# Optimization experiments

Hardware: AMD Instinct MI355X
Metric: run time of the kernel (lower is better)

The kernel has to match this reference:

```python
import jax, jax.numpy as jnp
import numpy as np

B_, L, DM = 4, 1024, 1024
DI, DS, DR, DC = 1024, 16, 64, 4
NH = 4
DK = DM // NH


def setup_inputs() -> dict:
    key = jax.random.key(0)
    ks = jax.random.split(key, 16)
    def w(i, shape, scale=0.02):
        return jax.random.normal(ks[i], shape, dtype=jnp.float32) * scale
    inp = {
        "x": jax.random.normal(ks[0], (B_, L, DM), dtype=jnp.float32),
        "xx": jax.random.normal(ks[1], (B_, L, DI), dtype=jnp.float32),
        "in_proj_w": w(2, (DI, DM)),
        "conv_w": w(3, (DI, 1, DC)),            # depthwise conv, groups=DI
        "conv_b": jnp.zeros((DI,), jnp.float32),
        "x_proj_w": w(4, (DR + 2 * DS, DI)),
        "dt_proj_w": w(5, (DI, DR)),
        "dt_proj_b": jnp.zeros((DI,), jnp.float32),
        "A_log": jnp.log(jnp.tile(jnp.arange(1, DS + 1, dtype=jnp.float32)[None, :], (DI, 1))),
        "D": jnp.ones((DI,), jnp.float32),
        "wq": w(6, (DM, DM)), "bq": jnp.zeros((DM,), jnp.float32),
        "wk": w(7, (DM, DM)), "bk": jnp.zeros((DM,), jnp.float32),
        "wv": w(8, (DM, DM)), "bv": jnp.zeros((DM,), jnp.float32),
        "wo": w(9, (DM, DM)), "bo": jnp.zeros((DM,), jnp.float32),
    }
    return inp


def _stim_forward(x, xx, in_proj_w, conv_w, conv_b, x_proj_w, dt_proj_w, dt_proj_b,
                  A_log, D, wq, bq, wk, bk, wv, bv, wo, bo):
    b, l, _ = xx.shape
    # query branch: in_proj (Linear, no bias)
    q = x @ in_proj_w.T                                    # (b, l, DI)
    # kv branch: causal depthwise conv1d (padding d_conv-1, truncated to l)
    xc = jnp.transpose(xx, (0, 2, 1))                      # (b, DI, l)
    xc = jax.lax.conv_general_dilated(
        xc, conv_w, window_strides=(1,), padding=[(DC - 1, 0)],
        dimension_numbers=("NCH", "OIH", "NCH"), feature_group_count=DI)
    xc = xc + conv_b[None, :, None]
    u = jax.nn.silu(jnp.transpose(xc, (0, 2, 1)))          # (b, l, DI)
    # SSM parameter projections
    A = -jnp.exp(A_log)                                    # (DI, DS)
    x_dbl = u @ x_proj_w.T                                 # (b, l, DR+2*DS)
    delta, Bm, Cm = jnp.split(x_dbl, [DR, DR + DS], axis=-1)
    delta = jax.nn.softplus(delta @ dt_proj_w.T + dt_proj_b)  # (b, l, DI)
    deltaA = jnp.exp(jnp.einsum("bld,dn->bldn", delta, A))    # (b, l, DI, DS)
    deltaBu = jnp.einsum("bld,bln,bld->bldn", delta, Bm, u)   # (b, l, DI, DS)
    # selective scan over time
    def step(h, inp):
        dA_t, dBu_t, C_t = inp
        h = dA_t * h + dBu_t                               # (b, DI, DS)
        y_t = jnp.einsum("bdn,bn->bd", h, C_t)             # (b, DI)
        return h, y_t
    h0 = jnp.zeros((b, DI, DS), dtype=u.dtype)
    _, ys = jax.lax.scan(step, h0, (jnp.moveaxis(deltaA, 1, 0),
                                    jnp.moveaxis(deltaBu, 1, 0),
                                    jnp.moveaxis(Cm, 1, 0)))
    y = jnp.moveaxis(ys, 0, 1) + u * D                     # (b, l, DI)
    # cross attention: query = q, key/value = y
    Q = (q @ wq.T + bq).reshape(b, l, NH, DK).transpose(0, 2, 1, 3)
    K = (y @ wk.T + bk).reshape(b, l, NH, DK).transpose(0, 2, 1, 3)
    V = (y @ wv.T + bv).reshape(b, l, NH, DK).transpose(0, 2, 1, 3)
    scale = 1.0 / np.sqrt(DK).astype(np.float32)
    scores = jnp.einsum("bhqd,bhkd->bhqk", Q, K) * scale
    attn = jax.nn.softmax(scores, axis=-1)
    out = jnp.einsum("bhqk,bhkd->bhqd", attn, V)
    out = out.transpose(0, 2, 1, 3).reshape(b, l, DM)
    return out @ wo.T + bo


def reference(x, xx, in_proj_w, conv_w, conv_b, x_proj_w, dt_proj_w, dt_proj_b,
              A_log, D, wq, bq, wk, bk, wv, bv, wo, bo):
    return _stim_forward(x, xx, in_proj_w, conv_w, conv_b, x_proj_w, dt_proj_w,
                         dt_proj_b, A_log, D, wq, bq, wk, bk, wv, bv, wo, bo)
```

## Files before the change

### kernel.cpp

```cpp
#include <hip/hip_runtime.h>
#include <math.h>

#define B_  4
#define L_  1024
#define DM  1024
#define DI  1024
#define DS  16
#define DR  64
#define DCV 4
#define NH  4
#define DK  256

#define NCH 32
#define CHL (L_ / NCH)

typedef __attribute__((ext_vector_type(8))) short short8;
typedef __attribute__((ext_vector_type(4))) float floatx4;

static __device__ __forceinline__ unsigned short f2bf(float f) {
    unsigned int u = __float_as_uint(f);
    u += 0x7fffu + ((u >> 16) & 1u);
    return (unsigned short)(u >> 16);
}
static __device__ __forceinline__ float bf2f(unsigned short s) {
    return __uint_as_float(((unsigned int)s) << 16);
}

#define GLL(gp, lp) __builtin_amdgcn_global_load_lds( \
        (const __attribute__((address_space(1))) void*)(gp), \
        (__attribute__((address_space(3))) void*)(lp), 16, 0, 0)

struct PrepArgs {
    const float* xx; const float* cw; const float* cb;
    float* u; unsigned short* ub;
    const float* xs; unsigned short* xd;
    const float* s[7]; unsigned short* d[7];
    int n[7];
    int ns[7];
};

__global__ __launch_bounds__(256) void prep(PrepArgs pa)
{
    int bid = blockIdx.x, tid = threadIdx.x;
    if (bid < 16384) {
        int idx = bid * 256 + tid;
        int d = idx & (DI - 1);
        int l = (idx >> 10) & (L_ - 1);
        int b = idx >> 20;
        const float* xb = pa.xx + (size_t)b * L_ * DI + d;
        float z = pa.cb[d];
#pragma unroll
        for (int j = 0; j < DCV; j++) {
            int t = l - (DCV - 1) + j;
            if (t >= 0) z += xb[(size_t)t * DI] * pa.cw[d * DCV + j];
        }
        float v = z / (1.0f + __expf(-z));
        pa.u[idx] = v;
        pa.ub[idx] = f2bf(v);
        return;
    }
    bid -= 16384;
    if (bid < 4096) {
        int i = (bid * 256 + tid) * 4;
        float4 v = *(const float4*)(pa.xs + i);
        ushort4 o;
        o.x = f2bf(v.x); o.y = f2bf(v.y); o.z = f2bf(v.z); o.w = f2bf(v.w);
        *(ushort4*)(pa.xd + i) = o;
        return;
    }
    bid -= 4096;
#pragma unroll
    for (int r = 0; r < 7; r++) {
        int nb = pa.n[r] >> 10;
        if (bid < nb) {
            int i = (bid * 256 + tid) * 4;
            int ns = pa.ns[r];
            const float* s = pa.s[r];
            ushort4 o;
            if (i + 4 <= ns) {
                float4 v = *(const float4*)(s + i);
                o.x = f2bf(v.x); o.y = f2bf(v.y); o.z = f2bf(v.z); o.w = f2bf(v.w);
            } else {
                float v[4];
#pragma unroll
                for (int j = 0; j < 4; j++) v[j] = (i + j < ns) ? s[i + j] : 0.f;
                o.x = f2bf(v[0]); o.y = f2bf(v[1]); o.z = f2bf(v[2]); o.w = f2bf(v[3]);
            }
            *(ushort4*)(pa.d[r] + i) = o;
            return;
        }
        bid -= nb;
    }
}

struct GDesc {
    const unsigned short* A;
    const unsigned short* W;
    const float* bias;
    float* Cf;
    unsigned short* Cb;
    int K, lda, ldw, ldc, ldc2;
    int mode;
    float scale;
    int gx, gy;
};
struct GArgs { GDesc g[3]; };

__global__ __launch_bounds__(256) void gemm_multi(GArgs ga)
{
    GDesc g = ga.g[blockIdx.z];
    if ((int)blockIdx.x >= g.gx || (int)blockIdx.y >= g.gy) return;

    __shared__ __align__(16) unsigned short Asm[2][128 * 32];
    __shared__ __align__(16) unsigned short Bsm[2][128 * 32];

    int tid = threadIdx.x;
    int wid = tid >> 6;
    int lane = tid & 63;
    int wm = wid & 1, wn = wid >> 1;
    int lr = lane & 15, quad = lane >> 4;

    const unsigned short* Ab = g.A + (size_t)blockIdx.y * 128 * g.lda;
    const unsigned short* Wb = g.W + (size_t)blockIdx.x * 128 * g.ldw;

    int srow = tid >> 2;
    int scol = (tid & 3) * 8;
    const unsigned short* Ap = Ab + (size_t)srow * g.lda + scol;
    const unsigned short* Wp = Wb + (size_t)srow * g.ldw + scol;

    int lbase = (wid * 16) * 32;

    floatx4 acc[4][4];
#pragma unroll
    for (int i = 0; i < 4; i++)
#pragma unroll
        for (int j = 0; j < 4; j++) acc[i][j] = (floatx4){0.f, 0.f, 0.f, 0.f};

    GLL(Ap, &Asm[0][lbase]);
    GLL(Ap + (size_t)64 * g.lda, &Asm[0][lbase + 64 * 32]);
    GLL(Wp, &Bsm[0][lbase]);
    GLL(Wp + (size_t)64 * g.ldw, &Bsm[0][lbase + 64 * 32]);
    Ap += 32; Wp += 32;
    __syncthreads();

    int cur = 0;
    for (int k0 = 0; k0 < g.K; k0 += 32) {
        int nxt = cur ^ 1;
        if (k0 + 32 < g.K) {
            GLL(Ap, &Asm[nxt][lbase]);
            GLL(Ap + (size_t)64 * g.lda, &Asm[nxt][lbase + 64 * 32]);
            GLL(Wp, &Bsm[nxt][lbase]);
            GLL(Wp + (size_t)64 * g.ldw, &Bsm[nxt][lbase + 64 * 32]);
            Ap += 32; Wp += 32;
        }

        short8 af[4], bf[4];
#pragma unroll
        for (int mt = 0; mt < 4; mt++)
            af[mt] = *(const short8*)&Asm[cur][(wm * 64 + mt * 16 + lr) * 32 + quad * 8];
#pragma unroll
        for (int nt = 0; nt < 4; nt++)
            bf[nt] = *(const short8*)&Bsm[cur][(wn * 64 + nt * 16 + lr) * 32 + quad * 8];
#pragma unroll
        for (int mt = 0; mt < 4; mt++)
#pragma unroll
            for (int nt = 0; nt < 4; nt++)
                acc[mt][nt] = __builtin_amdgcn_mfma_f32_16x16x32_bf16(
                    af[mt], bf[nt], acc[mt][nt], 0, 0, 0);
        __syncthreads();
        cur = nxt;
    }

    int bm = blockIdx.y * 128, bn = blockIdx.x * 128;
    int m = g.mode & 3;
#pragma unroll
    for (int mt = 0; mt < 4; mt++) {
#pragma unroll
        for (int nt = 0; nt < 4; nt++) {
            int row0 = bm + wm * 64 + mt * 16 + quad * 4;
            int col = bn + wn * 64 + nt * 16 + lr;
            float bv = g.bias ? g.bias[col] : 0.f;
#pragma unroll
            for (int i = 0; i < 4; i++) {
                float v = acc[mt][nt][i] * g.scale + bv;
                if (g.mode & 4) v = (v > 15.f) ? v : log1pf(__expf(v));
                if (m == 0) {
                    g.Cf[(size_t)(row0 + i) * g.ldc + col] = v;
                } else if (m == 1) {
                    g.Cb[(size_t)(row0 + i) * g.ldc + col] = f2bf(v);
                } else {
                    g.Cf[(size_t)(row0 + i) * g.ldc + col] = v;
                    g.Cb[(size_t)(row0 + i) * g.ldc2 + col] = f2bf(v);
                }
            }
        }
    }
}

__global__ __launch_bounds__(256) void gemm_batched(
    const unsigned short* __restrict__ A, const unsigned short* __restrict__ W,
    unsigned short* __restrict__ C,
    int K, int lda, int ldw, int ldc,
    long long sA1, long long sA2, long long sW1, long long sW2,
    long long sC1, long long sC2, float scale)
{
    __shared__ __align__(16) unsigned short Asm[2][128 * 32];
    __shared__ __align__(16) unsigned short Bsm[2][128 * 32];

    int z = blockIdx.z;
    long long bq = z >> 2, hq = z & 3;
    int tid = threadIdx.x;
    int wid = tid >> 6;
    int lane = tid & 63;
    int wm = wid & 1, wn = wid >> 1;
    int lr = lane & 15, quad = lane >> 4;

    const unsigned short* Ab = A + bq * sA1 + hq * sA2 + (size_t)blockIdx.y * 128 * lda;
    const unsigned short* Wb = W + bq * sW1 + hq * sW2 + (size_t)blockIdx.x * 128 * ldw;

    int srow = tid >> 2;
    int scol = (tid & 3) * 8;
    const unsigned short* Ap = Ab + (size_t)srow * lda + scol;
    const unsigned short* Wp = Wb + (size_t)srow * ldw + scol;

    int lbase = (wid * 16) * 32;

    floatx4 acc[4][4];
#pragma unroll
    for (int i = 0; i < 4; i++)
#pragma unroll
        for (int j = 0; j < 4; j++) acc[i][j] = (floatx4){0.f, 0.f, 0.f, 0.f};

    GLL(Ap, &Asm[0][lbase]);
    GLL(Ap + (size_t)64 * lda, &Asm[0][lbase + 64 * 32]);
    GLL(Wp, &Bsm[0][lbase]);
    GLL(Wp + (size_t)64 * ldw, &Bsm[0][lbase + 64 * 32]);
    Ap += 32; Wp += 32;
    __syncthreads();

    int cur = 0;
    for (int k0 = 0; k0 < K; k0 += 32) {
        int nxt = cur ^ 1;
        if (k0 + 32 < K) {
            GLL(Ap, &Asm[nxt][lbase]);
            GLL(Ap + (size_t)64 * lda, &Asm[nxt][lbase + 64 * 32]);
            GLL(Wp, &Bsm[nxt][lbase]);
            GLL(Wp + (size_t)64 * ldw, &Bsm[nxt][lbase + 64 * 32]);
            Ap += 32; Wp += 32;
        }

        short8 af[4], bf[4];
#pragma unroll
        for (int mt = 0; mt < 4; mt++)
            af[mt] = *(const short8*)&Asm[cur][(wm * 64 + mt * 16 + lr) * 32 + quad * 8];
#pragma unroll
        for (int nt = 0; nt < 4; nt++)
            bf[nt] = *(const short8*)&Bsm[cur][(wn * 64 + nt * 16 + lr) * 32 + quad * 8];
#pragma unroll
        for (int mt = 0; mt < 4; mt++)
#pragma unroll
            for (int nt = 0; nt < 4; nt++)
                acc[mt][nt] = __builtin_amdgcn_mfma_f32_16x16x32_bf16(
                    af[mt], bf[nt], acc[mt][nt], 0, 0, 0);
        __syncthreads();
        cur = nxt;
    }

    long long coff = bq * sC1 + hq * sC2;
    int bm = blockIdx.y * 128, bn = blockIdx.x * 128;
    unsigned short* Cb = C + coff;

#pragma unroll
    for (int mt = 0; mt < 4; mt++) {
#pragma unroll
        for (int nt = 0; nt < 4; nt++) {
            int row0 = bm + wm * 64 + mt * 16 + quad * 4;
            int col = bn + wn * 64 + nt * 16 + lr;
#pragma unroll
            for (int i = 0; i < 4; i++)
                Cb[(size_t)(row0 + i) * ldc + col] = f2bf(acc[mt][nt][i] * scale);
        }
    }
}

__global__ __launch_bounds__(256) void scan_a(
    const float* __restrict__ delta, const float* __restrict__ u,
    const float* __restrict__ xdbl, const float* __restrict__ A_log,
    float* __restrict__ Hc, float* __restrict__ sumdv)
{
    int gid = blockIdx.x * 256 + threadIdx.x;
    int c = gid >> 12;
    int bd = gid & 4095;
    int b = bd >> 10, d = bd & 1023;

    float a[16];
#pragma unroll
    for (int j = 0; j < 4; j++) {
        float4 al = *(const float4*)(A_log + d * 16 + j * 4);
        a[j * 4 + 0] = -__expf(al.x); a[j * 4 + 1] = -__expf(al.y);
        a[j * 4 + 2] = -__expf(al.z); a[j * 4 + 3] = -__expf(al.w);
    }
    float h[16];
#pragma unroll
    for (int n = 0; n < 16; n++) h[n] = 0.f;
    float sd = 0.f;

    int t0 = c * CHL;
    const float* dp = delta + ((size_t)(b * L_) + t0) * DI + d;
    const float* up = u + ((size_t)(b * L_) + t0) * DI + d;
    const float* xp = xdbl + ((size_t)(b * L_) + t0) * 128;

#pragma unroll 4
    for (int t = 0; t < CHL; t++) {
        float dv = dp[t * DI];
        float uv = up[t * DI];
        float duv = dv * uv;
        sd += dv;
        float Bv[16];
#pragma unroll
        for (int j = 0; j < 4; j++) {
            float4 bq = *(const float4*)(xp + t * 128 + 64 + j * 4);
            Bv[j * 4 + 0] = bq.x; Bv[j * 4 + 1] = bq.y;
            Bv[j * 4 + 2] = bq.z; Bv[j * 4 + 3] = bq.w;
        }
#pragma unroll
        for (int n = 0; n < 16; n++)
            h[n] = __expf(dv * a[n]) * h[n] + duv * Bv[n];
    }

    float* hp = Hc + ((size_t)c * 4096 + bd) * 16;
#pragma unroll
    for (int j = 0; j < 4; j++)
        *(float4*)(hp + j * 4) = make_float4(h[j * 4], h[j * 4 + 1], h[j * 4 + 2], h[j * 4 + 3]);
    sumdv[c * 4096 + bd] = sd;
}

__global__ __launch_bounds__(256) void scan_b(
    float* __restrict__ Hc, const float* __restrict__ sumdv,
    const float* __restrict__ A_log)
{
    int bd = blockIdx.x * 256 + threadIdx.x;
    int d = bd & 1023;

    float a[16];
#pragma unroll
    for (int j = 0; j < 4; j++) {
        float4 al = *(const float4*)(A_log + d * 16 + j * 4);
        a[j * 4 + 0] = -__expf(al.x); a[j * 4 + 1] = -__expf(al.y);
        a[j * 4 + 2] = -__expf(al.z); a[j * 4 + 3] = -__expf(al.w);
    }
    float H[16];
#pragma unroll
    for (int n = 0; n < 16; n++) H[n] = 0.f;

    for (int c = 0; c < NCH; c++) {
        float* hp = Hc + ((size_t)c * 4096 + bd) * 16;
        float sdv = sumdv[c * 4096 + bd];
        float hc[16];
#pragma unroll
        for (int j = 0; j < 4; j++) {
            float4 q = *(const float4*)(hp + j * 4);
            hc[j * 4 + 0] = q.x; hc[j * 4 + 1] = q.y; hc[j * 4 + 2] = q.z; hc[j * 4 + 3] = q.w;
        }
#pragma unroll
        for (int j = 0; j < 4; j++)
            *(float4*)(hp + j * 4) = make_float4(H[j * 4], H[j * 4 + 1], H[j * 4 + 2], H[j * 4 + 3]);
#pragma unroll
        for (int n = 0; n < 16; n++)
            H[n] = __expf(a[n] * sdv) * H[n] + hc[n];
    }
}

__global__ __launch_bounds__(256) void scan_c(
    const float* __restrict__ delta, const float* __restrict__ u,
    const float* __restrict__ xdbl, const float* __restrict__ A_log,
    const float* __restrict__ Dv, const float* __restrict__ Hstart,
    unsigned short* __restrict__ y)
{
    int gid = blockIdx.x * 256 + threadIdx.x;
    int c = gid >> 12;
    int bd = gid & 4095;
    int b = bd >> 10, d = bd & 1023;

    float a[16];
#pragma unroll
    for (int j = 0; j < 4; j++) {
        float4 al = *(const float4*)(A_log + d * 16 + j * 4);
        a[j * 4 + 0] = -__expf(al.x); a[j * 4 + 1] = -__expf(al.y);
        a[j * 4 + 2] = -__expf(al.z); a[j * 4 + 3] = -__expf(al.w);
    }
    float h[16];
    const float* hp = Hstart + ((size_t)c * 4096 + bd) * 16;
#pragma unroll
    for (int j = 0; j < 4; j++) {
        float4 q = *(const float4*)(hp + j * 4);
        h[j * 4 + 0] = q.x; h[j * 4 + 1] = q.y; h[j * 4 + 2] = q.z; h[j * 4 + 3] = q.w;
    }
    float Dd = Dv[d];

    int t0 = c * CHL;
    const float* dp = delta + ((size_t)(b * L_) + t0) * DI + d;
    const float* up = u + ((size_t)(b * L_) + t0) * DI + d;
    const float* xp = xdbl + ((size_t)(b * L_) + t0) * 128;
    unsigned short* yp = y + ((size_t)(b * L_) + t0) * DI + d;

#pragma unroll 4
    for (int t = 0; t < CHL; t++) {
        float dv = dp[t * DI];
        float uv = up[t * DI];
        float duv = dv * uv;
        float Bv[16], Cv[16];
#pragma unroll
        for (int j = 0; j < 4; j++) {
            float4 bq = *(const float4*)(xp + t * 128 + 64 + j * 4);
            Bv[j * 4 + 0] = bq.x; Bv[j * 4 + 1] = bq.y;
            Bv[j * 4 + 2] = bq.z; Bv[j * 4 + 3] = bq.w;
            float4 cq = *(const float4*)(xp + t * 128 + 80 + j * 4);
            Cv[j * 4 + 0] = cq.x; Cv[j * 4 + 1] = cq.y;
            Cv[j * 4 + 2] = cq.z; Cv[j * 4 + 3] = cq.w;
        }
        float ys = 0.f;
#pragma unroll
        for (int n = 0; n < 16; n++) {
            h[n] = __expf(dv * a[n]) * h[n] + duv * Bv[n];
            ys += h[n] * Cv[n];
        }
        yp[t * DI] = f2bf(ys + uv * Dd);
    }
}

__global__ __launch_bounds__(256) void softmax_rows(unsigned short* __restrict__ S)
{
    int row = blockIdx.x * 4 + (threadIdx.x >> 6);
    int lane = threadIdx.x & 63;
    unsigned short* p = S + (size_t)row * 1024;

    float v[16];
#pragma unroll
    for (int ch = 0; ch < 4; ch++) {
        ushort4 u4 = *(const ushort4*)(p + ch * 256 + lane * 4);
        v[ch * 4 + 0] = bf2f(u4.x); v[ch * 4 + 1] = bf2f(u4.y);
        v[ch * 4 + 2] = bf2f(u4.z); v[ch * 4 + 3] = bf2f(u4.w);
    }
    float m = -1e30f;
#pragma unroll
    for (int i = 0; i < 16; i++) m = fmaxf(m, v[i]);
#pragma unroll
    for (int off = 32; off >= 1; off >>= 1) m = fmaxf(m, __shfl_xor(m, off));
    float s = 0.f;
#pragma unroll
    for (int i = 0; i < 16; i++) { v[i] = __expf(v[i] - m); s += v[i]; }
#pragma unroll
    for (int off = 32; off >= 1; off >>= 1) s += __shfl_xor(s, off);
    float inv = 1.0f / s;
#pragma unroll
    for (int ch = 0; ch < 4; ch++) {
        ushort4 o;
        o.x = f2bf(v[ch * 4 + 0] * inv); o.y = f2bf(v[ch * 4 + 1] * inv);
        o.z = f2bf(v[ch * 4 + 2] * inv); o.w = f2bf(v[ch * 4 + 3] * inv);
        *(ushort4*)(p + ch * 256 + lane * 4) = o;
    }
}

__global__ __launch_bounds__(256) void transpose_v(
    const unsigned short* __restrict__ V, unsigned short* __restrict__ VT)
{
    __shared__ unsigned short tl[32][36];
    int bh = blockIdx.z;
    int b = bh >> 2, h = bh & 3;
    int l0 = blockIdx.x * 32, d0 = blockIdx.y * 32;
    int tid = threadIdx.x;
    int r = tid >> 3, c4 = (tid & 7) * 4;

    const unsigned short* src = V + ((size_t)(b * L_ + l0 + r)) * 1024 + h * DK + d0 + c4;
    ushort4 v = *(const ushort4*)src;
    tl[r][c4 + 0] = v.x; tl[r][c4 + 1] = v.y; tl[r][c4 + 2] = v.z; tl[r][c4 + 3] = v.w;
    __syncthreads();

    unsigned short* dst = VT + ((size_t)bh * DK + d0 + r) * L_ + l0 + c4;
    ushort4 o;
    o.x = tl[c4 + 0][r]; o.y = tl[c4 + 1][r]; o.z = tl[c4 + 2][r]; o.w = tl[c4 + 3][r];
    *(ushort4*)dst = o;
}

extern "C" void kernel_launch(void* const* d_in, const int* in_sizes, int n_in,
                              void* d_out, int out_size, void* d_ws, size_t ws_size,
                              hipStream_t stream)
{
    const float* x         = (const float*)d_in[0];
    const float* xx        = (const float*)d_in[1];
    const float* in_proj_w = (const float*)d_in[2];
    const float* conv_w    = (const float*)d_in[3];
    const float* conv_b    = (const float*)d_in[4];
    const float* x_proj_w  = (const float*)d_in[5];
    const float* dt_proj_w = (const float*)d_in[6];
    const float* dt_proj_b = (const float*)d_in[7];
    const float* A_log     = (const float*)d_in[8];
    const float* Dvec      = (const float*)d_in[9];
    const float* wq        = (const float*)d_in[10];
    const float* bq        = (const float*)d_in[11];
    const float* wk        = (const float*)d_in[12];
    const float* bk        = (const float*)d_in[13];
    const float* wv        = (const float*)d_in[14];
    const float* bv        = (const float*)d_in[15];
    const float* wo        = (const float*)d_in[16];
    const float* bo        = (const float*)d_in[17];
    float* out = (float*)d_out;

    char* w = (char*)d_ws;
    const size_t MB = 1024 * 1024, KB = 1024;
    float*          u_f    = (float*)(w + 0);
    float*          delta  = (float*)(w + 16 * MB);
    unsigned short* Sbuf   = (unsigned short*)(w + 0);
    unsigned short* x_bf   = (unsigned short*)(w + 32 * MB);
    unsigned short* Q_bf   = x_bf;
    unsigned short* q_bf   = (unsigned short*)(w + 40 * MB);
    unsigned short* VT     = q_bf;
    unsigned short* y_bf   = (unsigned short*)(w + 48 * MB);
    unsigned short* AO     = y_bf;
    unsigned short* K_bf   = (unsigned short*)(w + 56 * MB);
    unsigned short* V_bf   = (unsigned short*)(w + 64 * MB);
    unsigned short* u_bf   = (unsigned short*)(w + 72 * MB);
    float*          Hc     = (float*)(w + 72 * MB);
    float*          xdbl   = (float*)(w + 80 * MB);
    unsigned short* xdblb  = (unsigned short*)(w + 82 * MB);
    unsigned short* w_in   = (unsigned short*)(w + 83 * MB);
    unsigned short* w_q    = (unsigned short*)(w + 85 * MB);
    unsigned short* w_k    = (unsigned short*)(w + 87 * MB);
    unsigned short* w_v    = (unsigned short*)(w + 89 * MB);
    unsigned short* w_o    = (unsigned short*)(w + 91 * MB);
    unsigned short* w_xp   = (unsigned short*)(w + 93 * MB);
    unsigned short* w_dt   = (unsigned short*)(w + 93 * MB + 256 * KB);
    float*          sumdv  = (float*)(w + 93 * MB + 384 * KB);

    dim3 blk(256);
    const long long LL = L_;

    PrepArgs pa;
    pa.xx = xx; pa.cw = conv_w; pa.cb = conv_b; pa.u = u_f; pa.ub = u_bf;
    pa.xs = x; pa.xd = x_bf;
    pa.s[0] = in_proj_w; pa.d[0] = w_in; pa.n[0] = 1048576; pa.ns[0] = 1048576;
    pa.s[1] = wq;        pa.d[1] = w_q;  pa.n[1] = 1048576; pa.ns[1] = 1048576;
    pa.s[2] = wk;        pa.d[2] = w_k;  pa.n[2] = 1048576; pa.ns[2] = 1048576;
    pa.s[3] = wv;        pa.d[3] = w_v;  pa.n[3] = 1048576; pa.ns[3] = 1048576;
    pa.s[4] = wo;        pa.d[4] = w_o;  pa.n[4] = 1048576; pa.ns[4] = 1048576;
    pa.s[5] = x_proj_w;  pa.d[5] = w_xp; pa.n[5] = 131072;  pa.ns[5] = 98304;
    pa.s[6] = dt_proj_w; pa.d[6] = w_dt; pa.n[6] = 65536;   pa.ns[6] = 65536;
    prep<<<dim3(25792), blk, 0, stream>>>(pa);

    {
        GArgs ga = {};
        ga.g[0] = (GDesc){x_bf, w_in, nullptr, nullptr, q_bf,
                          1024, 1024, 1024, 1024, 0, 1, 1.0f, 8, 32};
        ga.g[1] = (GDesc){u_bf, w_xp, nullptr, xdbl, xdblb,
                          1024, 1024, 1024, 128, 128, 2, 1.0f, 1, 32};
        gemm_multi<<<dim3(8, 32, 2), blk, 0, stream>>>(ga);
    }
    {
        GArgs ga = {};
        ga.g[0] = (GDesc){xdblb, w_dt, dt_proj_b, delta, nullptr,
                          64, 128, 64, 1024, 0, 0 | 4, 1.0f, 8, 32};
        gemm_multi<<<dim3(8, 32, 1), blk, 0, stream>>>(ga);
    }
    scan_a<<<dim3(512), blk, 0, stream>>>(delta, u_f, xdbl, A_log, Hc, sumdv);
    scan_b<<<dim3(16), blk, 0, stream>>>(Hc, sumdv, A_log);
    scan_c<<<dim3(512), blk, 0, stream>>>(delta, u_f, xdbl, A_log, Dvec, Hc, y_bf);

    {
        GArgs ga = {};
        ga.g[0] = (GDesc){q_bf, w_q, bq, nullptr, Q_bf, 1024, 1024, 1024, 1024, 0, 1, 1.0f, 8, 32};
        ga.g[1] = (GDesc){y_bf, w_k, bk, nullptr, K_bf, 1024, 1024, 1024, 1024, 0, 1, 1.0f, 8, 32};
        ga.g[2] = (GDesc){y_bf, w_v, bv, nullptr, V_bf, 1024, 1024, 1024, 1024, 0, 1, 1.0f, 8, 32};
        gemm_multi<<<dim3(8, 32, 3), blk, 0, stream>>>(ga);
    }
    gemm_batched<<<dim3(8, 8, 16), blk, 0, stream>>>(Q_bf, K_bf, Sbuf,
        DK, 1024, 1024, 1024,
        LL * 1024, 256, LL * 1024, 256,
        4 * LL * 1024, LL * 1024, 0.0625f);
    softmax_rows<<<dim3(4096), blk, 0, stream>>>(Sbuf);
    transpose_v<<<dim3(32, 8, 16), blk, 0, stream>>>(V_bf, VT);
    gemm_batched<<<dim3(2, 8, 16), blk, 0, stream>>>(Sbuf, VT, AO,
        1024, 1024, 1024, 1024,
        4 * LL * 1024, LL * 1024,
        4 * (long long)DK * 1024, (long long)DK * 1024,
        LL * 1024, 256, 1.0f);
    {
        GArgs ga = {};
        ga.g[0] = (GDesc){AO, w_o, bo, out, nullptr, 1024, 1024, 1024, 1024, 0, 0, 1.0f, 8, 32};
        gemm_multi<<<dim3(8, 32, 1), blk, 0, stream>>>(ga);
    }
}
```

Baseline: 428.4 us.

## Triple-buffer GEMM K-loop with vmcnt waits and merge softmax/transpose launches

Both GEMM kernels move from a double-buffered K loop to a three-stage shared-memory pipeline. Two tiles are kept in flight, completion is tracked with explicit s_waitcnt vmcnt plus s_barrier, and the per-iteration __syncthreads after the MFMAs is dropped. The next stage's loads are issued after the fragment reads so they overlap the MFMAs. Separately, the softmax and V-transpose kernels are merged into one launch to save a kernel launch. The cost is 50% more LDS per block, which can lower occupancy, and the hand-written wait counts must match the number of outstanding loads.

```diff
diff --git a/kernel.cpp b/kernel.cpp
--- a/kernel.cpp
+++ b/kernel.cpp
@@ -111,8 +111,8 @@
     GDesc g = ga.g[blockIdx.z];
     if ((int)blockIdx.x >= g.gx || (int)blockIdx.y >= g.gy) return;
 
-    __shared__ __align__(16) unsigned short Asm[2][128 * 32];
-    __shared__ __align__(16) unsigned short Bsm[2][128 * 32];
+    __shared__ __align__(16) unsigned short Asm[3][128 * 32];
+    __shared__ __align__(16) unsigned short Bsm[3][128 * 32];
 
     int tid = threadIdx.x;
     int wid = tid >> 6;
@@ -136,23 +136,23 @@
 #pragma unroll
         for (int j = 0; j < 4; j++) acc[i][j] = (floatx4){0.f, 0.f, 0.f, 0.f};
 
-    GLL(Ap, &Asm[0][lbase]);
-    GLL(Ap + (size_t)64 * g.lda, &Asm[0][lbase + 64 * 32]);
-    GLL(Wp, &Bsm[0][lbase]);
-    GLL(Wp + (size_t)64 * g.ldw, &Bsm[0][lbase + 64 * 32]);
-    Ap += 32; Wp += 32;
-    __syncthreads();
-
-    int cur = 0;
-    for (int k0 = 0; k0 < g.K; k0 += 32) {
-        int nxt = cur ^ 1;
-        if (k0 + 32 < g.K) {
-            GLL(Ap, &Asm[nxt][lbase]);
-            GLL(Ap + (size_t)64 * g.lda, &Asm[nxt][lbase + 64 * 32]);
-            GLL(Wp, &Bsm[nxt][lbase]);
-            GLL(Wp + (size_t)64 * g.ldw, &Bsm[nxt][lbase + 64 * 32]);
-            Ap += 32; Wp += 32;
-        }
+#define STAGE_M(buf) do { \
+        GLL(Ap, &Asm[buf][lbase]); \
+        GLL(Ap + (size_t)64 * g.lda, &Asm[buf][lbase + 64 * 32]); \
+        GLL(Wp, &Bsm[buf][lbase]); \
+        GLL(Wp + (size_t)64 * g.ldw, &Bsm[buf][lbase + 64 * 32]); \
+        Ap += 32; Wp += 32; \
+    } while (0)
+
+    int nK = g.K >> 5;
+    STAGE_M(0);
+    if (nK > 1) STAGE_M(1);
+
+    int cur = 0, stg = 2;
+    for (int k = 0; k < nK - 1; k++) {
+        asm volatile("s_waitcnt vmcnt(4)" ::: "memory");
+        __builtin_amdgcn_s_barrier();
+        __builtin_amdgcn_sched_barrier(0);
 
         short8 af[4], bf[4];
 #pragma unroll
@@ -161,15 +161,40 @@
 #pragma unroll
         for (int nt = 0; nt < 4; nt++)
             bf[nt] = *(const short8*)&Bsm[cur][(wn * 64 + nt * 16 + lr) * 32 + quad * 8];
+
+        if (k + 2 < nK) {
+            STAGE_M(stg);
+            stg = (stg == 2) ? 0 : stg + 1;
+        }
+
 #pragma unroll
         for (int mt = 0; mt < 4; mt++)
 #pragma unroll
             for (int nt = 0; nt < 4; nt++)
                 acc[mt][nt] = __builtin_amdgcn_mfma_f32_16x16x32_bf16(
                     af[mt], bf[nt], acc[mt][nt], 0, 0, 0);
-        __syncthreads();
-        cur = nxt;
-    }
+        cur = (cur == 2) ? 0 : cur + 1;
+    }
+    {
+        asm volatile("s_waitcnt vmcnt(0)" ::: "memory");
+        __builtin_amdgcn_s_barrier();
+        __builtin_amdgcn_sched_barrier(0);
+
+        short8 af[4], bf[4];
+#pragma unroll
+        for (int mt = 0; mt < 4; mt++)
+            af[mt] = *(const short8*)&Asm[cur][(wm * 64 + mt * 16 + lr) * 32 + quad * 8];
+#pragma unroll
+        for (int nt = 0; nt < 4; nt++)
+            bf[nt] = *(const short8*)&Bsm[cur][(wn * 64 + nt * 16 + lr) * 32 + quad * 8];
+#pragma unroll
+        for (int mt = 0; mt < 4; mt++)
+#pragma unroll
+            for (int nt = 0; nt < 4; nt++)
+                acc[mt][nt] = __builtin_amdgcn_mfma_f32_16x16x32_bf16(
+                    af[mt], bf[nt], acc[mt][nt], 0, 0, 0);
+    }
+#undef STAGE_M
 
     int bm = blockIdx.y * 128, bn = blockIdx.x * 128;
     int m = g.mode & 3;
@@ -204,8 +229,8 @@
     long long sA1, long long sA2, long long sW1, long long sW2,
     long long sC1, long long sC2, float scale)
 {
-    __shared__ __align__(16) unsigned short Asm[2][128 * 32];
-    __shared__ __align__(16) unsigned short Bsm[2][128 * 32];
+    __shared__ __align__(16) unsigned short Asm[3][128 * 32];
+    __shared__ __align__(16) unsigned short Bsm[3][128 * 32];
 
     int z = blockIdx.z;
     long long bq = z >> 2, hq = z & 3;
@@ -231,23 +256,23 @@
 #pragma unroll
         for (int j = 0; j < 4; j++) acc[i][j] = (floatx4){0.f, 0.f, 0.f, 0.f};
 
-    GLL(Ap, &Asm[0][lbase]);
-    GLL(Ap + (size_t)64 * lda, &Asm[0][lbase + 64 * 32]);
-    GLL(Wp, &Bsm[0][lbase]);
-    GLL(Wp + (size_t)64 * ldw, &Bsm[0][lbase + 64 * 32]);
-    Ap += 32; Wp += 32;
-    __syncthreads();
-
-    int cur = 0;
-    for (int k0 = 0; k0 < K; k0 += 32) {
-        int nxt = cur ^ 1;
-        if (k0 + 32 < K) {
-            GLL(Ap, &Asm[nxt][lbase]);
-            GLL(Ap + (size_t)64 * lda, &Asm[nxt][lbase + 64 * 32]);
-            GLL(Wp, &Bsm[nxt][lbase]);
-            GLL(Wp + (size_t)64 * ldw, &Bsm[nxt][lbase + 64 * 32]);
-            Ap += 32; Wp += 32;
-        }
+#define STAGE_B(buf) do { \
+        GLL(Ap, &Asm[buf][lbase]); \
+        GLL(Ap + (size_t)64 * lda, &Asm[buf][lbase + 64 * 32]); \
+        GLL(Wp, &Bsm[buf][lbase]); \
+        GLL(Wp + (size_t)64 * ldw, &Bsm[buf][lbase + 64 * 32]); \
+        Ap += 32; Wp += 32; \
+    } while (0)
+
+    int nK = K >> 5;
+    STAGE_B(0);
+    if (nK > 1) STAGE_B(1);
+
+    int cur = 0, stg = 2;
+    for (int k = 0; k < nK - 1; k++) {
+        asm volatile("s_waitcnt vmcnt(4)" ::: "memory");
+        __builtin_amdgcn_s_barrier();
+        __builtin_amdgcn_sched_barrier(0);
 
         short8 af[4], bf[4];
 #pragma unroll
@@ -256,15 +281,40 @@
 #pragma unroll
         for (int nt = 0; nt < 4; nt++)
             bf[nt] = *(const short8*)&Bsm[cur][(wn * 64 + nt * 16 + lr) * 32 + quad * 8];
+
+        if (k + 2 < nK) {
+            STAGE_B(stg);
+            stg = (stg == 2) ? 0 : stg + 1;
+        }
+
 #pragma unroll
         for (int mt = 0; mt < 4; mt++)
 #pragma unroll
             for (int nt = 0; nt < 4; nt++)
                 acc[mt][nt] = __builtin_amdgcn_mfma_f32_16x16x32_bf16(
                     af[mt], bf[nt], acc[mt][nt], 0, 0, 0);
-        __syncthreads();
-        cur = nxt;
-    }
+        cur = (cur == 2) ? 0 : cur + 1;
+    }
+    {
+        asm volatile("s_waitcnt vmcnt(0)" ::: "memory");
+        __builtin_amdgcn_s_barrier();
+        __builtin_amdgcn_sched_barrier(0);
+
+        short8 af[4], bf[4];
+#pragma unroll
+        for (int mt = 0; mt < 4; mt++)
+            af[mt] = *(const short8*)&Asm[cur][(wm * 64 + mt * 16 + lr) * 32 + quad * 8];
+#pragma unroll
+        for (int nt = 0; nt < 4; nt++)
+            bf[nt] = *(const short8*)&Bsm[cur][(wn * 64 + nt * 16 + lr) * 32 + quad * 8];
+#pragma unroll
+        for (int mt = 0; mt < 4; mt++)
+#pragma unroll
+            for (int nt = 0; nt < 4; nt++)
+                acc[mt][nt] = __builtin_amdgcn_mfma_f32_16x16x32_bf16(
+                    af[mt], bf[nt], acc[mt][nt], 0, 0, 0);
+    }
+#undef STAGE_B
 
     long long coff = bq * sC1 + hq * sC2;
     int bm = blockIdx.y * 128, bn = blockIdx.x * 128;
@@ -429,46 +479,50 @@
     }
 }
 
-__global__ __launch_bounds__(256) void softmax_rows(unsigned short* __restrict__ S)
-{
-    int row = blockIdx.x * 4 + (threadIdx.x >> 6);
-    int lane = threadIdx.x & 63;
-    unsigned short* p = S + (size_t)row * 1024;
-
-    float v[16];
-#pragma unroll
-    for (int ch = 0; ch < 4; ch++) {
-        ushort4 u4 = *(const ushort4*)(p + ch * 256 + lane * 4);
-        v[ch * 4 + 0] = bf2f(u4.x); v[ch * 4 + 1] = bf2f(u4.y);
-        v[ch * 4 + 2] = bf2f(u4.z); v[ch * 4 + 3] = bf2f(u4.w);
-    }
-    float m = -1e30f;
-#pragma unroll
-    for (int i = 0; i < 16; i++) m = fmaxf(m, v[i]);
-#pragma unroll
-    for (int off = 32; off >= 1; off >>= 1) m = fmaxf(m, __shfl_xor(m, off));
-    float s = 0.f;
-#pragma unroll
-    for (int i = 0; i < 16; i++) { v[i] = __expf(v[i] - m); s += v[i]; }
-#pragma unroll
-    for (int off = 32; off >= 1; off >>= 1) s += __shfl_xor(s, off);
-    float inv = 1.0f / s;
-#pragma unroll
-    for (int ch = 0; ch < 4; ch++) {
-        ushort4 o;
-        o.x = f2bf(v[ch * 4 + 0] * inv); o.y = f2bf(v[ch * 4 + 1] * inv);
-        o.z = f2bf(v[ch * 4 + 2] * inv); o.w = f2bf(v[ch * 4 + 3] * inv);
-        *(ushort4*)(p + ch * 256 + lane * 4) = o;
-    }
-}
-
-__global__ __launch_bounds__(256) void transpose_v(
+__global__ __launch_bounds__(256) void softmax_transpose(
+    unsigned short* __restrict__ S,
     const unsigned short* __restrict__ V, unsigned short* __restrict__ VT)
 {
     __shared__ unsigned short tl[32][36];
-    int bh = blockIdx.z;
+    int bid = blockIdx.x;
+    if (bid < 4096) {
+        int row = bid * 4 + (threadIdx.x >> 6);
+        int lane = threadIdx.x & 63;
+        unsigned short* p = S + (size_t)row * 1024;
+
+        float v[16];
+#pragma unroll
+        for (int ch = 0; ch < 4; ch++) {
+            ushort4 u4 = *(const ushort4*)(p + ch * 256 + lane * 4);
+            v[ch * 4 + 0] = bf2f(u4.x); v[ch * 4 + 1] = bf2f(u4.y);
+            v[ch * 4 + 2] = bf2f(u4.z); v[ch * 4 + 3] = bf2f(u4.w);
+        }
+        float m = -1e30f;
+#pragma unroll
+        for (int i = 0; i < 16; i++) m = fmaxf(m, v[i]);
+#pragma unroll
+        for (int off = 32; off >= 1; off >>= 1) m = fmaxf(m, __shfl_xor(m, off));
+        float s = 0.f;
+#pragma unroll
+        for (int i = 0; i < 16; i++) { v[i] = __expf(v[i] - m); s += v[i]; }
+#pragma unroll
+        for (int off = 32; off >= 1; off >>= 1) s += __shfl_xor(s, off);
+        float inv = 1.0f / s;
+#pragma unroll
+        for (int ch = 0; ch < 4; ch++) {
+            ushort4 o;
+            o.x = f2bf(v[ch * 4 + 0] * inv); o.y = f2bf(v[ch * 4 + 1] * inv);
+            o.z = f2bf(v[ch * 4 + 2] * inv); o.w = f2bf(v[ch * 4 + 3] * inv);
+            *(ushort4*)(p + ch * 256 + lane * 4) = o;
+        }
+        return;
+    }
+    int tb = bid - 4096;
+    int bh = tb >> 8;
+    int rem = tb & 255;
+    int d0 = (rem >> 5) * 32;
+    int l0 = (rem & 31) * 32;
     int b = bh >> 2, h = bh & 3;
-    int l0 = blockIdx.x * 32, d0 = blockIdx.y * 32;
     int tid = threadIdx.x;
     int r = tid >> 3, c4 = (tid & 7) * 4;
 
@@ -577,8 +631,7 @@
         DK, 1024, 1024, 1024,
         LL * 1024, 256, LL * 1024, 256,
         4 * LL * 1024, LL * 1024, 0.0625f);
-    softmax_rows<<<dim3(4096), blk, 0, stream>>>(Sbuf);
-    transpose_v<<<dim3(32, 8, 16), blk, 0, stream>>>(V_bf, VT);
+    softmax_transpose<<<dim3(8192), blk, 0, stream>>>(Sbuf, V_bf, VT);
     gemm_batched<<<dim3(2, 8, 16), blk, 0, stream>>>(Sbuf, VT, AO,
         1024, 1024, 1024, 1024,
         4 * LL * 1024, LL * 1024,
```

Measured after the change: 402.7 us. 1.06x faster.
